# Optimization experiments

Measured on AMD Instinct MI355X. Metric: run time of the kernel, lower is better.

The kernel has to match this reference:

```python
import jax, jax.numpy as jnp
import numpy as np
from jax import lax

N, C_IN, C_OUT, H, W = 64, 192, 192, 64, 64
K, STRIDE, DILATION = 3, 1, 2
PAD = (K - 1) * DILATION // 2  # = 2, matches torch forward's explicit padding
BN_EPS = 1e-5


def setup_inputs() -> dict:
    key = jax.random.key(0)
    k1, k2, k3 = jax.random.split(key, 3)
    x = jax.random.normal(k1, (N, C_IN, H, W), dtype=jnp.float32)
    dw_w = jax.random.normal(k2, (C_IN, 1, K, K), dtype=jnp.float32) * 0.1
    pw_w = jax.random.normal(k3, (C_OUT, C_IN), dtype=jnp.float32) * 0.05
    gamma = jnp.ones((C_OUT,), dtype=jnp.float32)
    beta = jnp.zeros((C_OUT,), dtype=jnp.float32)
    return {"x": x, "dw_w": dw_w, "pw_w": pw_w, "gamma": gamma, "beta": beta}


def reference(x, dw_w, pw_w, gamma, beta):
    # ReLU
    h = jax.nn.relu(x)
    # Depthwise dilated conv: groups == C_in, no bias
    y = lax.conv_general_dilated(
        h, dw_w,
        window_strides=(STRIDE, STRIDE),
        padding=((PAD, PAD), (PAD, PAD)),
        rhs_dilation=(DILATION, DILATION),
        dimension_numbers=("NCHW", "OIHW", "NCHW"),
        feature_group_count=C_IN,
    )
    # Pointwise 1x1 conv == per-pixel GEMM over channels
    z = jnp.einsum("nchw,oc->nohw", y, pw_w)
    # BatchNorm2d in training mode: batch statistics over (N, H, W)
    mean = jnp.mean(z, axis=(0, 2, 3), keepdims=True)
    var = jnp.var(z, axis=(0, 2, 3), keepdims=True)
    zhat = (z - mean) * lax.rsqrt(var + BN_EPS)
    return zhat * gamma[None, :, None, None] + beta[None, :, None, None]
```

## Files before the change

### kernel.cpp

```cpp
#include <hip/hip_runtime.h>

#define N_    64
#define CIN   192
#define COUT  192
#define H_    64
#define W_    64
#define BN_EPS 1e-5f
#define M_    262144.0f
#define SYT_STRIDE 200
#define NCOPY 64

typedef __attribute__((ext_vector_type(8))) short  short8;
typedef __attribute__((ext_vector_type(4))) float  floatx4;

__device__ __forceinline__ unsigned short f2bf(float f) {
    union { float f; unsigned int u; } v; v.f = f;
    unsigned int u = v.u;
    return (unsigned short)((u + 0x7FFFu + ((u >> 16) & 1u)) >> 16);
}

#define SC_OFF 384
#define SH_OFF 576
#define CP_OFF 32768

__global__ __launch_bounds__(256) void init_ws(
    const float* __restrict__ pw, float* __restrict__ ws,
    unsigned short* __restrict__ pwb)
{
    const int b = blockIdx.x, t = threadIdx.x;
    if (b < 144) {
        const int i = b * 256 + t;
        pwb[i] = f2bf(pw[i]);
    } else {
        const int i = (b - 144) * 256 + t;
        ws[CP_OFF + i] = 0.f;
    }
}

__global__ __launch_bounds__(256) void dw_kernel(
    const float* __restrict__ x, const float* __restrict__ dww,
    unsigned short* __restrict__ y)
{
    __shared__ float sdw[CIN * 9];

    const int t   = threadIdx.x;
    const int bid = blockIdx.x;
    const int wg  = ((bid & 7) << 9) | (bid >> 3);
    const int n   = wg >> 6;
    const int h   = wg & 63;

    for (int i = t; i < CIN * 9; i += 256) sdw[i] = dww[i];

    const int  w    = t & 63;
    const int  cblk = t >> 6;
    const bool wm0  = (w >= 2);
    const bool wm2  = (w <= 61);
    __syncthreads();

    const int h0 = h - 2;
    for (int e = 0; e < 6; ++e) {
        const int cb = (cblk + (e << 2)) << 3;
        float a[8];
        #pragma unroll
        for (int ci = 0; ci < 8; ++ci) {
            const int c = cb + ci;
            const float* xp = x + (((size_t)(n * CIN + c)) << 12) + w;
            const float* kw = &sdw[c * 9];
            float acc = 0.f;
            #pragma unroll
            for (int dh = 0; dh < 3; ++dh) {
                const int hh = h0 + (dh << 1);
                if ((unsigned)hh < 64u) {
                    float v1 = fmaxf(xp[hh << 6], 0.f);
                    float v0 = __shfl_up(v1, 2, 64);
                    float v2 = __shfl_down(v1, 2, 64);
                    v0 = wm0 ? v0 : 0.f;
                    v2 = wm2 ? v2 : 0.f;
                    acc = fmaf(v0, kw[3 * dh + 0], acc);
                    acc = fmaf(v1, kw[3 * dh + 1], acc);
                    acc = fmaf(v2, kw[3 * dh + 2], acc);
                }
            }
            a[ci] = acc;
        }
        uint4 pk;
        pk.x = (unsigned)f2bf(a[0]) | ((unsigned)f2bf(a[1]) << 16);
        pk.y = (unsigned)f2bf(a[2]) | ((unsigned)f2bf(a[3]) << 16);
        pk.z = (unsigned)f2bf(a[4]) | ((unsigned)f2bf(a[5]) << 16);
        pk.w = (unsigned)f2bf(a[6]) | ((unsigned)f2bf(a[7]) << 16);
        *(uint4*)&y[(size_t)wg * 12288 + (size_t)w * 192 + cb] = pk;
    }
}

__global__ __launch_bounds__(256) void gemm_stats_kernel(
    const unsigned short* __restrict__ y, const unsigned short* __restrict__ pwb,
    float* __restrict__ ws)
{
    __shared__ unsigned short syT[W_ * SYT_STRIDE];

    const int t  = threadIdx.x;
    const int wg = blockIdx.x;

    const size_t ybase = (size_t)wg * 12288;
    #pragma unroll
    for (int it = 0; it < 6; ++it) {
        const int idx = it * 256 + t;
        const int px  = idx / 24;
        const int cb  = (idx % 24) << 3;
        uint4 v = *(const uint4*)&y[ybase + (size_t)idx * 8];
        *(uint4*)&syT[px * SYT_STRIDE + cb] = v;
    }
    __syncthreads();

    const int wv   = t >> 6;
    const int lane = t & 63;
    const int l15  = lane & 15;
    const int q    = lane >> 4;
    const int ob   = wv * 48;

    floatx4 acc[3][4];
    #pragma unroll
    for (int mt = 0; mt < 3; ++mt)
        #pragma unroll
        for (int nt = 0; nt < 4; ++nt) acc[mt][nt] = (floatx4)0.f;

    #pragma unroll
    for (int kk = 0; kk < 6; ++kk) {
        const int k0 = kk * 32 + q * 8;

        short8 af[3];
        #pragma unroll
        for (int mt = 0; mt < 3; ++mt)
            af[mt] = *(const short8*)&pwb[(size_t)(ob + mt * 16 + l15) * CIN + k0];

        short8 bf[4];
        #pragma unroll
        for (int nt = 0; nt < 4; ++nt)
            bf[nt] = *(const short8*)&syT[(nt * 16 + l15) * SYT_STRIDE + k0];

        #pragma unroll
        for (int mt = 0; mt < 3; ++mt)
            #pragma unroll
            for (int nt = 0; nt < 4; ++nt)
                acc[mt][nt] = __builtin_amdgcn_mfma_f32_16x16x32_bf16(
                    af[mt], bf[nt], acc[mt][nt], 0, 0, 0);
    }

    float* cp = ws + CP_OFF + (size_t)(wg & (NCOPY - 1)) * 384;
    #pragma unroll
    for (int mt = 0; mt < 3; ++mt) {
        #pragma unroll
        for (int r = 0; r < 4; ++r) {
            const int o = ob + mt * 16 + q * 4 + r;
            float s = 0.f, ss = 0.f;
            #pragma unroll
            for (int nt = 0; nt < 4; ++nt) {
                const float v = acc[mt][nt][r];
                s  += v;
                ss += v * v;
            }
            #pragma unroll
            for (int off = 8; off > 0; off >>= 1) {
                s  += __shfl_down(s,  off, 16);
                ss += __shfl_down(ss, off, 16);
            }
            if (l15 == 0) {
                atomicAdd(&cp[o], s);
                atomicAdd(&cp[192 + o], ss);
            }
        }
    }
}

__global__ __launch_bounds__(256) void stats2_kernel(
    const float* __restrict__ gamma, const float* __restrict__ beta,
    float* __restrict__ ws)
{
    int t = threadIdx.x;
    if (t < COUT) {
        float s = 0.f, ss = 0.f;
        for (int k = 0; k < NCOPY; ++k) {
            s  += ws[CP_OFF + k * 384 + t];
            ss += ws[CP_OFF + k * 384 + 192 + t];
        }
        const float invM = 1.0f / M_;
        float m    = s * invM;
        float v    = ss * invM - m * m;
        float rstd = rsqrtf(v + BN_EPS);
        float sc   = gamma[t] * rstd;
        ws[SC_OFF + t] = sc;
        ws[SH_OFF + t] = beta[t] - m * sc;
    }
}

__global__ __launch_bounds__(256) void gemm_norm_kernel(
    const unsigned short* __restrict__ y, const unsigned short* __restrict__ pwb,
    const float* __restrict__ ws, float* __restrict__ out)
{
    __shared__ unsigned short syT[W_ * SYT_STRIDE];

    const int t  = threadIdx.x;
    const int wg = blockIdx.x;
    const int n  = wg >> 6;
    const int h  = wg & 63;

    const size_t ybase = (size_t)wg * 12288;
    #pragma unroll
    for (int it = 0; it < 6; ++it) {
        const int idx = it * 256 + t;
        const int px  = idx / 24;
        const int cb  = (idx % 24) << 3;
        uint4 v = *(const uint4*)&y[ybase + (size_t)idx * 8];
        *(uint4*)&syT[px * SYT_STRIDE + cb] = v;
    }
    __syncthreads();

    const int wv   = t >> 6;
    const int lane = t & 63;
    const int l15  = lane & 15;
    const int q    = lane >> 4;
    const int ob   = wv * 48;

    floatx4 acc[3][4];
    #pragma unroll
    for (int mt = 0; mt < 3; ++mt)
        #pragma unroll
        for (int nt = 0; nt < 4; ++nt) acc[mt][nt] = (floatx4)0.f;

    #pragma unroll
    for (int kk = 0; kk < 6; ++kk) {
        const int k0 = kk * 32 + q * 8;

        short8 af[3];
        #pragma unroll
        for (int mt = 0; mt < 3; ++mt)
            af[mt] = *(const short8*)&pwb[(size_t)(ob + mt * 16 + l15) * CIN + k0];

        short8 bf[4];
        #pragma unroll
        for (int nt = 0; nt < 4; ++nt)
            bf[nt] = *(const short8*)&syT[(nt * 16 + l15) * SYT_STRIDE + k0];

        #pragma unroll
        for (int mt = 0; mt < 3; ++mt)
            #pragma unroll
            for (int nt = 0; nt < 4; ++nt)
                acc[mt][nt] = __builtin_amdgcn_mfma_f32_16x16x32_bf16(
                    af[mt], bf[nt], acc[mt][nt], 0, 0, 0);
    }

    const size_t base = (((size_t)n * COUT) << 12) + ((size_t)h << 6);
    #pragma unroll
    for (int mt = 0; mt < 3; ++mt) {
        #pragma unroll
        for (int r = 0; r < 4; ++r) {
            const int o  = ob + mt * 16 + q * 4 + r;
            const float sc = ws[SC_OFF + o];
            const float sh = ws[SH_OFF + o];
            #pragma unroll
            for (int nt = 0; nt < 4; ++nt) {
                const float v = fmaf(acc[mt][nt][r], sc, sh);
                out[base + ((size_t)o << 12) + nt * 16 + l15] = v;
            }
        }
    }
}

__global__ __launch_bounds__(384) void zero_ws(float* __restrict__ ws) {
    int t = threadIdx.x;
    if (t < 384) ws[t] = 0.f;
}

__global__ __launch_bounds__(256) void stats_kernel(
    const float* __restrict__ gamma, const float* __restrict__ beta,
    float* __restrict__ ws)
{
    int t = threadIdx.x;
    if (t < COUT) {
        const float invM = 1.0f / M_;
        float m    = ws[t] * invM;
        float v    = ws[COUT + t] * invM - m * m;
        float rstd = rsqrtf(v + BN_EPS);
        float sc   = gamma[t] * rstd;
        ws[2 * COUT + t] = sc;
        ws[3 * COUT + t] = beta[t] - m * sc;
    }
}

__global__ __launch_bounds__(256, 4) void fused_kernel(
    const float* __restrict__ x, const float* __restrict__ dww,
    const float* __restrict__ pw, float* __restrict__ zout,
    float* __restrict__ ws)
{
    __shared__ float  sdw[CIN * 9];
    __shared__ unsigned short syT[W_ * SYT_STRIDE];

    const int t = threadIdx.x;
    const int n = blockIdx.x >> 6;
    const int h = blockIdx.x & 63;

    for (int i = t; i < CIN * 9; i += 256) sdw[i] = dww[i];

    const int  w    = t & 63;
    const int  cblk = t >> 6;
    const bool wm0  = (w >= 2);
    const bool wm2  = (w <= 61);
    const int  om   = wm0 ? -2 : 0;
    const int  op   = wm2 ?  2 : 0;
    __syncthreads();

    for (int e = 0; e < 6; ++e) {
        const int cb = (cblk + (e << 2)) << 3;
        float a[8];
        #pragma unroll
        for (int ci = 0; ci < 8; ++ci) {
            const int c = cb + ci;
            const float* xr0 = x + (((size_t)(n * CIN + c)) << 12) + w;
            const float* kw  = &sdw[c * 9];
            float acc = 0.f;
            #pragma unroll
            for (int dh = 0; dh < 3; ++dh) {
                const int hh = h + 2 * dh - 2;
                if ((unsigned)hh < 64u) {
                    const float* xr = xr0 + (hh << 6);
                    float v0 = fmaxf(xr[om], 0.f);
                    float v1 = fmaxf(xr[0],  0.f);
                    float v2 = fmaxf(xr[op], 0.f);
                    v0 = wm0 ? v0 : 0.f;
                    v2 = wm2 ? v2 : 0.f;
                    acc = fmaf(v0, kw[3 * dh + 0], acc);
                    acc = fmaf(v1, kw[3 * dh + 1], acc);
                    acc = fmaf(v2, kw[3 * dh + 2], acc);
                }
            }
            a[ci] = acc;
        }
        uint4 pk;
        pk.x = (unsigned)f2bf(a[0]) | ((unsigned)f2bf(a[1]) << 16);
        pk.y = (unsigned)f2bf(a[2]) | ((unsigned)f2bf(a[3]) << 16);
        pk.z = (unsigned)f2bf(a[4]) | ((unsigned)f2bf(a[5]) << 16);
        pk.w = (unsigned)f2bf(a[6]) | ((unsigned)f2bf(a[7]) << 16);
        *(uint4*)&syT[w * SYT_STRIDE + cb] = pk;
    }
    __syncthreads();

    const int wv   = t >> 6;
    const int lane = t & 63;
    const int l15  = lane & 15;
    const int q    = lane >> 4;
    const int ob   = wv * 48;

    floatx4 acc[3][4];
    #pragma unroll
    for (int mt = 0; mt < 3; ++mt)
        #pragma unroll
        for (int nt = 0; nt < 4; ++nt) acc[mt][nt] = (floatx4)0.f;

    #pragma unroll
    for (int kk = 0; kk < 6; ++kk) {
        const int k0 = kk * 32 + q * 8;

        short8 af[3];
        #pragma unroll
        for (int mt = 0; mt < 3; ++mt) {
            const float4* ap = (const float4*)(pw + (size_t)(ob + mt * 16 + l15) * CIN + k0);
            float4 u = ap[0];
            float4 v = ap[1];
            short8 f;
            f[0] = (short)f2bf(u.x); f[1] = (short)f2bf(u.y);
            f[2] = (short)f2bf(u.z); f[3] = (short)f2bf(u.w);
            f[4] = (short)f2bf(v.x); f[5] = (short)f2bf(v.y);
            f[6] = (short)f2bf(v.z); f[7] = (short)f2bf(v.w);
            af[mt] = f;
        }

        short8 bf[4];
        #pragma unroll
        for (int nt = 0; nt < 4; ++nt)
            bf[nt] = *(const short8*)&syT[(nt * 16 + l15) * SYT_STRIDE + k0];

        #pragma unroll
        for (int mt = 0; mt < 3; ++mt)
            #pragma unroll
            for (int nt = 0; nt < 4; ++nt)
                acc[mt][nt] = __builtin_amdgcn_mfma_f32_16x16x32_bf16(
                    af[mt], bf[nt], acc[mt][nt], 0, 0, 0);
    }

    const size_t base = (((size_t)n * COUT) << 12) + ((size_t)h << 6);
    #pragma unroll
    for (int mt = 0; mt < 3; ++mt) {
        #pragma unroll
        for (int r = 0; r < 4; ++r) {
            const int o = ob + mt * 16 + q * 4 + r;
            float s = 0.f, ss = 0.f;
            #pragma unroll
            for (int nt = 0; nt < 4; ++nt) {
                const float v = acc[mt][nt][r];
                zout[base + ((size_t)o << 12) + nt * 16 + l15] = v;
                s  += v;
                ss += v * v;
            }
            #pragma unroll
            for (int off = 8; off > 0; off >>= 1) {
                s  += __shfl_down(s,  off, 16);
                ss += __shfl_down(ss, off, 16);
            }
            if (l15 == 0) {
                atomicAdd(&ws[o], s);
                atomicAdd(&ws[COUT + o], ss);
            }
        }
    }
}

__global__ __launch_bounds__(256) void norm_kernel(
    float* __restrict__ out, const float* __restrict__ ws)
{
    const size_t i = (size_t)blockIdx.x * 256 + threadIdx.x;
    const int c = (int)((i >> 10) % COUT);
    const float sc = ws[2 * COUT + c];
    const float sh = ws[3 * COUT + c];
    float4 v = ((const float4*)out)[i];
    v.x = fmaf(v.x, sc, sh);
    v.y = fmaf(v.y, sc, sh);
    v.z = fmaf(v.z, sc, sh);
    v.w = fmaf(v.w, sc, sh);
    ((float4*)out)[i] = v;
}

extern "C" void kernel_launch(void* const* d_in, const int* in_sizes, int n_in,
                              void* d_out, int out_size, void* d_ws, size_t ws_size,
                              hipStream_t stream) {
    const float* x     = (const float*)d_in[0];
    const float* dww   = (const float*)d_in[1];
    const float* pw    = (const float*)d_in[2];
    const float* gamma = (const float*)d_in[3];
    const float* beta  = (const float*)d_in[4];
    float* out = (float*)d_out;
    float* ws  = (float*)d_ws;

    const size_t PWB_OFF = 4096;
    const size_t Y_OFF   = 1u << 20;
    const size_t Y_BYTES = (size_t)N_ * H_ * W_ * CIN * 2;
    const size_t need    = Y_OFF + Y_BYTES;

    if (ws_size >= need) {
        unsigned short* pwb = (unsigned short*)((char*)d_ws + PWB_OFF);
        unsigned short* y   = (unsigned short*)((char*)d_ws + Y_OFF);

        init_ws<<<240, 256, 0, stream>>>(pw, ws, pwb);
        dw_kernel<<<N_ * H_, 256, 0, stream>>>(x, dww, y);
        gemm_stats_kernel<<<N_ * H_, 256, 0, stream>>>(y, pwb, ws);
        stats2_kernel<<<1, 256, 0, stream>>>(gamma, beta, ws);
        gemm_norm_kernel<<<N_ * H_, 256, 0, stream>>>(y, pwb, ws, out);
    } else {
        zero_ws<<<1, 384, 0, stream>>>(ws);
        fused_kernel<<<N_ * H_, 256, 0, stream>>>(x, dww, pw, out, ws);
        stats_kernel<<<1, 256, 0, stream>>>(gamma, beta, ws);
        norm_kernel<<<49152, 256, 0, stream>>>(out, ws);
    }
}
```

Measured before the change: 610.4 us.

## Restructure depthwise kernel to stream rows per channel group with register sliding window

The depthwise kernel now assigns each block to a batch image and an 8-channel group, not an (n,h) row. Each thread walks all 64 rows of two channels, keeping a rolling window of ReLU'd, shuffled rows in registers so every input element is loaded once rather than three times. Filter weights stay in registers, and results are staged through LDS and written as channel-blocked tiles (8 channels x 64 pixels). The two GEMM kernels' transpose loads change to match this new y layout. The exchange is a much smaller grid (1536 blocks) with a serial row loop and more register pressure.

After: 490.5 us. -19.6%, faster.

```diff
diff --git a/kernel.cpp b/kernel.cpp
--- a/kernel.cpp
+++ b/kernel.cpp
@@ -37,58 +37,127 @@
     }
 }
 
+#define PROC(vraw, t0, t1, t2) do {                    \
+    float _v = fmaxf((vraw), 0.f);                     \
+    float _u = __shfl_up(_v, 2, 64);                   \
+    float _d = __shfl_down(_v, 2, 64);                 \
+    (t0) = wm0 ? _u : 0.f;                             \
+    (t1) = _v;                                         \
+    (t2) = wm2 ? _d : 0.f; } while (0)
+
 __global__ __launch_bounds__(256) void dw_kernel(
     const float* __restrict__ x, const float* __restrict__ dww,
     unsigned short* __restrict__ y)
 {
-    __shared__ float sdw[CIN * 9];
-
-    const int t   = threadIdx.x;
-    const int bid = blockIdx.x;
-    const int wg  = ((bid & 7) << 9) | (bid >> 3);
-    const int n   = wg >> 6;
-    const int h   = wg & 63;
-
-    for (int i = t; i < CIN * 9; i += 256) sdw[i] = dww[i];
-
-    const int  w    = t & 63;
-    const int  cblk = t >> 6;
+    __shared__ unsigned short sy[8 * 512];
+
+    const int t     = threadIdx.x;
+    const int w     = t & 63;
+    const int cpair = t >> 6;
+    const int cg    = blockIdx.x;
+    const int n     = blockIdx.y;
     const bool wm0  = (w >= 2);
     const bool wm2  = (w <= 61);
-    __syncthreads();
-
-    const int h0 = h - 2;
-    for (int e = 0; e < 6; ++e) {
-        const int cb = (cblk + (e << 2)) << 3;
-        float a[8];
-        #pragma unroll
-        for (int ci = 0; ci < 8; ++ci) {
-            const int c = cb + ci;
-            const float* xp = x + (((size_t)(n * CIN + c)) << 12) + w;
-            const float* kw = &sdw[c * 9];
-            float acc = 0.f;
-            #pragma unroll
-            for (int dh = 0; dh < 3; ++dh) {
-                const int hh = h0 + (dh << 1);
-                if ((unsigned)hh < 64u) {
-                    float v1 = fmaxf(xp[hh << 6], 0.f);
-                    float v0 = __shfl_up(v1, 2, 64);
-                    float v2 = __shfl_down(v1, 2, 64);
-                    v0 = wm0 ? v0 : 0.f;
-                    v2 = wm2 ? v2 : 0.f;
-                    acc = fmaf(v0, kw[3 * dh + 0], acc);
-                    acc = fmaf(v1, kw[3 * dh + 1], acc);
-                    acc = fmaf(v2, kw[3 * dh + 2], acc);
-                }
-            }
-            a[ci] = acc;
-        }
-        uint4 pk;
-        pk.x = (unsigned)f2bf(a[0]) | ((unsigned)f2bf(a[1]) << 16);
-        pk.y = (unsigned)f2bf(a[2]) | ((unsigned)f2bf(a[3]) << 16);
-        pk.z = (unsigned)f2bf(a[4]) | ((unsigned)f2bf(a[5]) << 16);
-        pk.w = (unsigned)f2bf(a[6]) | ((unsigned)f2bf(a[7]) << 16);
-        *(uint4*)&y[(size_t)wg * 12288 + (size_t)w * 192 + cb] = pk;
+
+    const int c0 = cg * 8 + cpair * 2;
+
+    float kw[2][9];
+    #pragma unroll
+    for (int ch = 0; ch < 2; ++ch)
+        #pragma unroll
+        for (int i = 0; i < 9; ++i)
+            kw[ch][i] = dww[(c0 + ch) * 9 + i];
+
+    const float* xp[2];
+    xp[0] = x + (((size_t)(n * CIN + c0)) << 12) + w;
+    xp[1] = xp[0] + 4096;
+
+    float Pm[2][3], Pc[2][3], Pn[2][3], Qm[2][3], Qc[2][3], Qn[2][3];
+    float r0[2], r1[2];
+
+    #pragma unroll
+    for (int ch = 0; ch < 2; ++ch) {
+        Pm[ch][0] = Pm[ch][1] = Pm[ch][2] = 0.f;
+        Qm[ch][0] = Qm[ch][1] = Qm[ch][2] = 0.f;
+        float x0 = xp[ch][0];
+        float x1 = xp[ch][64];
+        float x2 = xp[ch][128];
+        float x3 = xp[ch][192];
+        r0[ch]   = xp[ch][256];
+        r1[ch]   = xp[ch][320];
+        PROC(x0, Pc[ch][0], Pc[ch][1], Pc[ch][2]);
+        PROC(x1, Qc[ch][0], Qc[ch][1], Qc[ch][2]);
+        PROC(x2, Pn[ch][0], Pn[ch][1], Pn[ch][2]);
+        PROC(x3, Qn[ch][0], Qn[ch][1], Qn[ch][2]);
+    }
+
+    const size_t tile0 = (size_t)(n * 64) * 12288 + (size_t)cg * 512;
+
+    #pragma unroll 4
+    for (int k = 0; k < 32; ++k) {
+        const int ra = 2 * k + 6, rb = 2 * k + 7;
+        float n0[2], n1[2];
+        #pragma unroll
+        for (int ch = 0; ch < 2; ++ch) {
+            n0[ch] = (ra < 64) ? xp[ch][ra << 6] : 0.f;
+            n1[ch] = (rb < 64) ? xp[ch][rb << 6] : 0.f;
+        }
+
+        float oa[2], ob[2];
+        #pragma unroll
+        for (int ch = 0; ch < 2; ++ch) {
+            float a = 0.f;
+            a = fmaf(Pm[ch][0], kw[ch][0], a);
+            a = fmaf(Pm[ch][1], kw[ch][1], a);
+            a = fmaf(Pm[ch][2], kw[ch][2], a);
+            a = fmaf(Pc[ch][0], kw[ch][3], a);
+            a = fmaf(Pc[ch][1], kw[ch][4], a);
+            a = fmaf(Pc[ch][2], kw[ch][5], a);
+            a = fmaf(Pn[ch][0], kw[ch][6], a);
+            a = fmaf(Pn[ch][1], kw[ch][7], a);
+            a = fmaf(Pn[ch][2], kw[ch][8], a);
+            oa[ch] = a;
+            float b = 0.f;
+            b = fmaf(Qm[ch][0], kw[ch][0], b);
+            b = fmaf(Qm[ch][1], kw[ch][1], b);
+            b = fmaf(Qm[ch][2], kw[ch][2], b);
+            b = fmaf(Qc[ch][0], kw[ch][3], b);
+            b = fmaf(Qc[ch][1], kw[ch][4], b);
+            b = fmaf(Qc[ch][2], kw[ch][5], b);
+            b = fmaf(Qn[ch][0], kw[ch][6], b);
+            b = fmaf(Qn[ch][1], kw[ch][7], b);
+            b = fmaf(Qn[ch][2], kw[ch][8], b);
+            ob[ch] = b;
+        }
+        const unsigned d0 = (unsigned)f2bf(oa[0]) | ((unsigned)f2bf(oa[1]) << 16);
+        const unsigned d1 = (unsigned)f2bf(ob[0]) | ((unsigned)f2bf(ob[1]) << 16);
+        const int slot = (2 * k) & 7;
+        const int si   = w * 8 + cpair * 2;
+        *(unsigned int*)&sy[slot * 512 + si]       = d0;
+        *(unsigned int*)&sy[(slot + 1) * 512 + si] = d1;
+
+        #pragma unroll
+        for (int ch = 0; ch < 2; ++ch) {
+            #pragma unroll
+            for (int i = 0; i < 3; ++i) { Pm[ch][i] = Pc[ch][i]; Pc[ch][i] = Pn[ch][i]; }
+            PROC(r0[ch], Pn[ch][0], Pn[ch][1], Pn[ch][2]);
+            #pragma unroll
+            for (int i = 0; i < 3; ++i) { Qm[ch][i] = Qc[ch][i]; Qc[ch][i] = Qn[ch][i]; }
+            PROC(r1[ch], Qn[ch][0], Qn[ch][1], Qn[ch][2]);
+            r0[ch] = n0[ch];
+            r1[ch] = n1[ch];
+        }
+
+        if ((k & 3) == 3) {
+            __syncthreads();
+            const int hb = (k >> 2) << 3;
+            const unsigned u0 = t, u1 = t + 256;
+            uint4 v0 = *(const uint4*)&sy[u0 * 8];
+            uint4 v1 = *(const uint4*)&sy[u1 * 8];
+            *(uint4*)&y[tile0 + (size_t)(hb + (u0 >> 6)) * 12288 + (u0 & 63) * 8] = v0;
+            *(uint4*)&y[tile0 + (size_t)(hb + (u1 >> 6)) * 12288 + (u1 & 63) * 8] = v1;
+            __syncthreads();
+        }
     }
 }
 
@@ -105,8 +174,8 @@
     #pragma unroll
     for (int it = 0; it < 6; ++it) {
         const int idx = it * 256 + t;
-        const int px  = idx / 24;
-        const int cb  = (idx % 24) << 3;
+        const int px  = idx & 63;
+        const int cb  = (idx >> 6) << 3;
         uint4 v = *(const uint4*)&y[ybase + (size_t)idx * 8];
         *(uint4*)&syT[px * SYT_STRIDE + cb] = v;
     }
@@ -208,8 +277,8 @@
     #pragma unroll
     for (int it = 0; it < 6; ++it) {
         const int idx = it * 256 + t;
-        const int px  = idx / 24;
-        const int cb  = (idx % 24) << 3;
+        const int px  = idx & 63;
+        const int cb  = (idx >> 6) << 3;
         uint4 v = *(const uint4*)&y[ybase + (size_t)idx * 8];
         *(uint4*)&syT[px * SYT_STRIDE + cb] = v;
     }
@@ -316,7 +385,7 @@
         for (int ci = 0; ci < 8; ++ci) {
             const int c = cb + ci;
             const float* xr0 = x + (((size_t)(n * CIN + c)) << 12) + w;
-            const float* kw  = &sdw[c * 9];
+            const float* kwp = &sdw[c * 9];
             float acc = 0.f;
             #pragma unroll
             for (int dh = 0; dh < 3; ++dh) {
@@ -328,9 +397,9 @@
                     float v2 = fmaxf(xr[op], 0.f);
                     v0 = wm0 ? v0 : 0.f;
                     v2 = wm2 ? v2 : 0.f;
-                    acc = fmaf(v0, kw[3 * dh + 0], acc);
-                    acc = fmaf(v1, kw[3 * dh + 1], acc);
-                    acc = fmaf(v2, kw[3 * dh + 2], acc);
+                    acc = fmaf(v0, kwp[3 * dh + 0], acc);
+                    acc = fmaf(v1, kwp[3 * dh + 1], acc);
+                    acc = fmaf(v2, kwp[3 * dh + 2], acc);
                 }
             }
             a[ci] = acc;
@@ -450,7 +519,7 @@
         unsigned short* y   = (unsigned short*)((char*)d_ws + Y_OFF);
 
         init_ws<<<240, 256, 0, stream>>>(pw, ws, pwb);
-        dw_kernel<<<N_ * H_, 256, 0, stream>>>(x, dww, y);
+        dw_kernel<<<dim3(24, 64), 256, 0, stream>>>(x, dww, y);
         gemm_stats_kernel<<<N_ * H_, 256, 0, stream>>>(y, pwb, ws);
         stats2_kernel<<<1, 256, 0, stream>>>(gamma, beta, ws);
         gemm_norm_kernel<<<N_ * H_, 256, 0, stream>>>(y, pwb, ws, out);
```
